# Kernel tuning notes

Hardware: AMD Instinct MI355X
Metric: run time of the kernel (lower is better)

## Reference

```python
import jax, jax.numpy as jnp
import numpy as np

# NF4 codebook (bitsandbytes normal-float-4 values)
NF4 = jnp.asarray(np.array([
    -1.0, -0.6961928009986877, -0.5250730514526367, -0.39491748809814453,
    -0.28444138169288635, -0.18477343022823334, -0.09105003625154495, 0.0,
    0.07958029955625534, 0.16093020141124725, 0.24611230194568634, 0.33791524171829224,
    0.44070982933044434, 0.5626170039176941, 0.7229568362236023, 1.0], dtype=np.float32))

BLOCK = 64         # bnb nf4 blocksize
SCALING = 2.0      # alpha / r = 128 / 64
OUT, IN = 4096, 4096

def dequantize_nf4(codes, absmax):
    # codes: [out, in] int32 in [0,16); absmax: [out*in/BLOCK] per-block scale
    vals = NF4[codes].reshape(-1, BLOCK)           # [n_blocks, BLOCK]
    w = vals * absmax[:, None]                     # blockwise rescale
    return w.reshape(OUT, IN)                      # [out, in]

def setup_inputs() -> dict:
    key = jax.random.key(0)
    k1, k2, k3, k4, k5 = jax.random.split(key, 5)
    x = jax.random.normal(k1, (4, 2048, 4096), dtype=jnp.float32)
    lora_A = jax.random.normal(k2, (64, 4096), dtype=jnp.float32) * 0.02
    lora_B = jax.random.normal(k3, (4096, 64), dtype=jnp.float32) * 0.02
    absmax = jax.random.uniform(k4, (4096 * 4096 // BLOCK,), dtype=jnp.float32) * 0.1
    qweight_codes = jax.random.randint(k5, (4096, 4096), 0, 16, dtype=jnp.int32)
    return {"x": x, "lora_A": lora_A, "lora_B": lora_B,
            "absmax": absmax, "qweight_codes": qweight_codes}

def reference(x, lora_A, lora_B, absmax, qweight_codes):
    # LinearForward, quantized nf4 path, no dora/bone, dropout disabled (eval):
    # F.linear(x, W) + scaling * F.linear(F.linear(x, lora_A), lora_B)
    W = dequantize_nf4(qweight_codes, absmax)              # [out, in]
    base = jnp.einsum('btd,od->bto', x, W)                 # base GEMM
    lora = jnp.einsum('btr,or->bto', jnp.einsum('btd,rd->btr', x, lora_A), lora_B)
    return base + SCALING * lora
```

## Files before the change

### kernel.cpp

```cpp
#include <hip/hip_runtime.h>


typedef _Float16 half8 __attribute__((ext_vector_type(8)));
typedef float f32x4 __attribute__((ext_vector_type(4)));

#define M_DIM 8192
#define N_DIM 4096
#define K_DIM 4096
#define NT (K_DIM / 64)

__constant__ float NF4C[16] = {
    -1.0f, -0.6961928009986877f, -0.5250730514526367f, -0.39491748809814453f,
    -0.28444138169288635f, -0.18477343022823334f, -0.09105003625154495f, 0.0f,
    0.07958029955625534f, 0.16093020141124725f, 0.24611230194568634f, 0.33791524171829224f,
    0.44070982933044434f, 0.5626170039176941f, 0.7229568362236023f, 1.0f};

__device__ __forceinline__ void gl16(void* lds_p, const void* g) {
  __builtin_amdgcn_global_load_lds(
      (const __attribute__((address_space(1))) void*)g,
      (__attribute__((address_space(3))) void*)lds_p, 16, 0, 0);
}

__global__ __launch_bounds__(256) void prep_x(const float4* __restrict__ x,
                                              half8* __restrict__ xh) {
  size_t i = (size_t)blockIdx.x * 256 + threadIdx.x;
  float4 a = x[2 * i];
  float4 b = x[2 * i + 1];
  half8 h;
  h[0] = (_Float16)a.x; h[1] = (_Float16)a.y; h[2] = (_Float16)a.z; h[3] = (_Float16)a.w;
  h[4] = (_Float16)b.x; h[5] = (_Float16)b.y; h[6] = (_Float16)b.z; h[7] = (_Float16)b.w;
  xh[i] = h;
}

#define PWP 132
__global__ __launch_bounds__(256) void prep_w(const float* __restrict__ lora_A,
                                              const float* __restrict__ lora_B,
                                              const float* __restrict__ absmax,
                                              const int* __restrict__ codes,
                                              _Float16* __restrict__ Wc) {
  __shared__ float At[64 * PWP];
  __shared__ float Bt[64 * PWP];
  __shared__ float nf4s[16];
  const int tid = threadIdx.x;
  const int bxi = blockIdx.x & 31;
  const int byo = blockIdx.x >> 5;
  const int i0 = bxi * 128;
  const int o0 = byo * 128;
  if (tid < 16) nf4s[tid] = NF4C[tid];
  for (int idx = tid; idx < 8192; idx += 256) {
    int r = idx >> 7, ii = idx & 127;
    At[r * PWP + ii] = lora_A[(size_t)r * 4096 + i0 + ii];
  }
  for (int idx = tid; idx < 8192; idx += 256) {
    int oo = idx >> 6, r = idx & 63;
    Bt[r * PWP + oo] = lora_B[(size_t)(o0 + oo) * 64 + r];
  }
  __syncthreads();
  const int tx = tid & 15;
  const int ty = tid >> 4;
  float accw[8][8];
#pragma unroll
  for (int i = 0; i < 8; ++i)
#pragma unroll
    for (int j = 0; j < 8; ++j) accw[i][j] = 0.0f;
  for (int r = 0; r < 64; ++r) {
    float4 a0 = *(const float4*)&At[r * PWP + tx * 8];
    float4 a1 = *(const float4*)&At[r * PWP + tx * 8 + 4];
    float4 b0 = *(const float4*)&Bt[r * PWP + ty * 8];
    float4 b1 = *(const float4*)&Bt[r * PWP + ty * 8 + 4];
    float av[8] = {a0.x, a0.y, a0.z, a0.w, a1.x, a1.y, a1.z, a1.w};
    float bv[8] = {b0.x, b0.y, b0.z, b0.w, b1.x, b1.y, b1.z, b1.w};
#pragma unroll
    for (int i = 0; i < 8; ++i)
#pragma unroll
      for (int j = 0; j < 8; ++j) accw[i][j] += bv[i] * av[j];
  }
#pragma unroll
  for (int i = 0; i < 8; ++i) {
    const int o_g = o0 + ty * 8 + i;
    const int* crow = codes + (size_t)o_g * 4096 + i0 + tx * 8;
    int4 c0 = *(const int4*)crow;
    int4 c1 = *(const int4*)(crow + 4);
    const float am = absmax[o_g * 64 + (i0 >> 6) + (tx >> 3)];
    half8 h;
    h[0] = (_Float16)(nf4s[c0.x] * am + 2.0f * accw[i][0]);
    h[1] = (_Float16)(nf4s[c0.y] * am + 2.0f * accw[i][1]);
    h[2] = (_Float16)(nf4s[c0.z] * am + 2.0f * accw[i][2]);
    h[3] = (_Float16)(nf4s[c0.w] * am + 2.0f * accw[i][3]);
    h[4] = (_Float16)(nf4s[c1.x] * am + 2.0f * accw[i][4]);
    h[5] = (_Float16)(nf4s[c1.y] * am + 2.0f * accw[i][5]);
    h[6] = (_Float16)(nf4s[c1.z] * am + 2.0f * accw[i][6]);
    h[7] = (_Float16)(nf4s[c1.w] * am + 2.0f * accw[i][7]);
    *(half8*)(Wc + (size_t)o_g * 4096 + i0 + tx * 8) = h;
  }
}


#define BAR __builtin_amdgcn_s_barrier()
#define PRIO1 __builtin_amdgcn_s_setprio(1)
#define PRIO0 __builtin_amdgcn_s_setprio(0)
#define SB0 __builtin_amdgcn_sched_barrier(0)

#define VMC_(N) asm volatile("s_waitcnt vmcnt(" #N ")" ::: "memory")
#define VMC(N) VMC_(N)
#define LG_(N)                                              \
  do {                                                      \
    asm volatile("s_waitcnt lgkmcnt(" #N ")" ::: "memory"); \
    __builtin_amdgcn_sched_barrier(0);                      \
  } while (0)
#define LG(N) LG_(N)

__global__ __launch_bounds__(512, 2) void gemm(const _Float16* __restrict__ Xh,
                                               const _Float16* __restrict__ Wc,
                                               float* __restrict__ out) {
  __shared__ _Float16 lds[65536];
  const int tid = threadIdx.x;
  const int lane = tid & 63;
  const int w = tid >> 6;

  const int swz = (blockIdx.x & 7) * 64 + (blockIdx.x >> 3);
  const int by = swz >> 4;
  const int bx = swz & 15;

  const int m16 = lane & 15;
  const int quad = lane >> 4;
  const int csw = (quad ^ (m16 & 7)) * 8;
  const int aoff0 = m16 * 64 + csw;
  const int aoff1 = m16 * 64 + (csw ^ 32);
  const int ha = w >> 2;
  const int hboff = ((w & 3) >> 1) * 8192 + (w & 1) * 4096;

  const int r0 = tid >> 3;
  const int lc = (tid & 7) ^ (r0 & 7);
  const _Float16* gAbase = Xh + (size_t)(by * 256 + r0) * K_DIM + lc * 8;
  const _Float16* gBbase = Wc + (size_t)(bx * 256 + r0) * K_DIM + lc * 8;

#define STAGE_A(H, BUF, T)                                                \
  do {                                                                    \
    _Float16* d_ = lds + (BUF) * 32768 + (H) * 8192 + w * 512;            \
    const _Float16* s_ = gAbase + (size_t)((H) * 128) * K_DIM + (T) * 64; \
    gl16(d_, s_);                                                         \
    gl16(d_ + 4096, s_ + (size_t)64 * K_DIM);                             \
  } while (0)
#define STAGE_B(H, BUF, T)                                                \
  do {                                                                    \
    _Float16* d_ = lds + (BUF) * 32768 + 16384 + (H) * 8192 + w * 512;    \
    const _Float16* s_ = gBbase + (size_t)((H) * 128) * K_DIM + (T) * 64; \
    gl16(d_, s_);                                                         \
    gl16(d_ + 4096, s_ + (size_t)64 * K_DIM);                             \
  } while (0)

  f32x4 acc[8][4];
#pragma unroll
  for (int m = 0; m < 8; ++m)
#pragma unroll
    for (int n = 0; n < 4; ++n) acc[m][n] = (f32x4){0.f, 0.f, 0.f, 0.f};

  half8 af[4][2];
  half8 bf[2][2];

#define RDA(FM, P)                                          \
  do {                                                      \
    af[FM][0] = *(const half8*)((P) + (FM)*1024 + aoff0);   \
    af[FM][1] = *(const half8*)((P) + (FM)*1024 + aoff1);   \
  } while (0)
#define RDB(FN, P)                                          \
  do {                                                      \
    bf[FN][0] = *(const half8*)((P) + (FN)*1024 + aoff0);   \
    bf[FN][1] = *(const half8*)((P) + (FN)*1024 + aoff1);   \
  } while (0)

#define MFM(FM, MH, NH)                                                      \
  do {                                                                       \
    acc[(MH)*4 + (FM)][(NH)*2 + 0] = __builtin_amdgcn_mfma_f32_16x16x32_f16( \
        af[FM][0], bf[0][0], acc[(MH)*4 + (FM)][(NH)*2 + 0], 0, 0, 0);       \
    acc[(MH)*4 + (FM)][(NH)*2 + 0] = __builtin_amdgcn_mfma_f32_16x16x32_f16( \
        af[FM][1], bf[0][1], acc[(MH)*4 + (FM)][(NH)*2 + 0], 0, 0, 0);       \
    acc[(MH)*4 + (FM)][(NH)*2 + 1] = __builtin_amdgcn_mfma_f32_16x16x32_f16( \
        af[FM][0], bf[1][0], acc[(MH)*4 + (FM)][(NH)*2 + 1], 0, 0, 0);       \
    acc[(MH)*4 + (FM)][(NH)*2 + 1] = __builtin_amdgcn_mfma_f32_16x16x32_f16( \
        af[FM][1], bf[1][1], acc[(MH)*4 + (FM)][(NH)*2 + 1], 0, 0, 0);       \
  } while (0)

#define MFN(FN, MH, NH)                                                          \
  do {                                                                           \
    _Pragma("unroll") for (int fm_ = 0; fm_ < 4; ++fm_) {                        \
      acc[(MH)*4 + fm_][(NH)*2 + (FN)] = __builtin_amdgcn_mfma_f32_16x16x32_f16( \
          af[fm_][0], bf[FN][0], acc[(MH)*4 + fm_][(NH)*2 + (FN)], 0, 0, 0);     \
      acc[(MH)*4 + fm_][(NH)*2 + (FN)] = __builtin_amdgcn_mfma_f32_16x16x32_f16( \
          af[fm_][1], bf[FN][1], acc[(MH)*4 + fm_][(NH)*2 + (FN)], 0, 0, 0);     \
    }                                                                            \
  } while (0)

#define TILE1(BUF, T, S)                                                \
  do {                                                                  \
    const _Float16* rA = lds + (BUF)*32768 + ha * 8192;                 \
    const _Float16* rB = lds + (BUF)*32768 + 16384 + hboff;             \
                   \
    RDB(0, rB); RDB(1, rB);                                             \
    RDA(0, rA); RDA(1, rA); RDA(2, rA); RDA(3, rA);                     \
    if (S) {                      \
      STAGE_A(0, (BUF) ^ 1, (T) + 1);                                   \
      STAGE_A(1, (BUF) ^ 1, (T) + 1);                                   \
      STAGE_B(0, (BUF) ^ 1, (T) + 1);                                   \
      STAGE_B(1, (BUF) ^ 1, (T) + 1);                                   \
    }                                                                   \
     \
    PRIO1;                                                              \
    LG(6); MFM(0, 0, 0);                             \
    LG(4); MFM(1, 0, 0);                                                \
    LG(2); MFM(2, 0, 0);                                                \
    LG(0); MFM(3, 0, 0);                                                \
    PRIO0;                                                              \
       \
    RDB(0, rB + 2048); RDB(1, rB + 2048);                               \
    PRIO1;                                                              \
    LG(2); MFN(0, 0, 1);                                                \
    LG(0); MFN(1, 0, 1);                                                \
    PRIO0;                                                              \
          \
    RDA(0, rA + 4096); RDA(1, rA + 4096);                               \
    RDA(2, rA + 4096); RDA(3, rA + 4096);                               \
    PRIO1;                                                              \
    LG(6); MFM(0, 1, 1);                                                \
    LG(4); MFM(1, 1, 1);                                                \
    LG(2); MFM(2, 1, 1);                                                \
    LG(0); MFM(3, 1, 1);                                                \
    PRIO0;                                                              \
        \
    RDB(0, rB); RDB(1, rB);                                             \
    PRIO1;                                                              \
    LG(2); MFN(0, 1, 0);                                                \
    LG(0); MFN(1, 1, 0);                                                \
    PRIO0;                                                              \
        \
    VMC(0);                                                             \
    BAR;                                                                \
  } while (0)

  STAGE_A(0, 0, 0);
  STAGE_A(1, 0, 0);
  STAGE_B(0, 0, 0);
  STAGE_B(1, 0, 0);
  VMC(0);
  BAR;

  for (int t2 = 0; t2 < NT - 2; t2 += 2) {
    TILE1(0, t2, 1);
    TILE1(1, t2 + 1, 1);
  }
  TILE1(0, NT - 2, 1);
  TILE1(1, NT - 1, 0);

  const size_t rowbase = (size_t)by * 256 + ha * 128 + quad * 4;
  const int colbase = bx * 256 + (w & 3) * 64 + m16;
#pragma unroll
  for (int m = 0; m < 8; ++m) {
#pragma unroll
    for (int r = 0; r < 4; ++r) {
      float* po = out + (rowbase + m * 16 + r) * N_DIM + colbase;
      po[0]  = acc[m][0][r];
      po[16] = acc[m][1][r];
      po[32] = acc[m][2][r];
      po[48] = acc[m][3][r];
    }
  }
}

extern "C" void kernel_launch(void* const* d_in, const int* in_sizes, int n_in,
                              void* d_out, int out_size, void* d_ws, size_t ws_size,
                              hipStream_t stream) {
  const float* x      = (const float*)d_in[0];
  const float* lora_A = (const float*)d_in[1];
  const float* lora_B = (const float*)d_in[2];
  const float* absmax = (const float*)d_in[3];
  const int*   codes  = (const int*)d_in[4];
  float* out = (float*)d_out;

  _Float16* Xh = (_Float16*)d_ws;
  _Float16* Wc = Xh + (size_t)M_DIM * K_DIM;

  hipLaunchKernelGGL(prep_x, dim3((M_DIM * K_DIM) / (8 * 256)), dim3(256), 0, stream,
                     (const float4*)x, (half8*)Xh);
  hipLaunchKernelGGL(prep_w, dim3((N_DIM / 128) * (K_DIM / 128)), dim3(256), 0, stream,
                     lora_A, lora_B, absmax, codes, Wc);
  hipLaunchKernelGGL(gemm, dim3((M_DIM / 256) * (N_DIM / 256)), dim3(512), 0, stream,
                     Xh, Wc, out);
}
```

Baseline: 534.6 us.

## Switch GEMM inner loop from 16x16x32 to 32x32x16 MFMA tiles

```diff
diff --git a/kernel.cpp b/kernel.cpp
--- a/kernel.cpp
+++ b/kernel.cpp
@@ -2,7 +2,7 @@
 
 
 typedef _Float16 half8 __attribute__((ext_vector_type(8)));
-typedef float f32x4 __attribute__((ext_vector_type(4)));
+typedef float f32x16 __attribute__((ext_vector_type(16)));
 
 #define M_DIM 8192
 #define N_DIM 4096
@@ -99,7 +99,6 @@
 #define BAR __builtin_amdgcn_s_barrier()
 #define PRIO1 __builtin_amdgcn_s_setprio(1)
 #define PRIO0 __builtin_amdgcn_s_setprio(0)
-#define SB0 __builtin_amdgcn_sched_barrier(0)
 
 #define VMC_(N) asm volatile("s_waitcnt vmcnt(" #N ")" ::: "memory")
 #define VMC(N) VMC_(N)
@@ -122,11 +121,14 @@
   const int by = swz >> 4;
   const int bx = swz & 15;
 
-  const int m16 = lane & 15;
-  const int quad = lane >> 4;
-  const int csw = (quad ^ (m16 & 7)) * 8;
-  const int aoff0 = m16 * 64 + csw;
-  const int aoff1 = m16 * 64 + (csw ^ 32);
+  const int l31 = lane & 31;
+  const int kh = lane >> 5;
+  const int rb = l31 & 7;
+  const int aro = l31 * 64;
+  const int ck0 = ((0 | kh) ^ rb) * 8;
+  const int ck1 = ((2 | kh) ^ rb) * 8;
+  const int ck2 = ((4 | kh) ^ rb) * 8;
+  const int ck3 = ((6 | kh) ^ rb) * 8;
   const int ha = w >> 2;
   const int hboff = ((w & 3) >> 1) * 8192 + (w & 1) * 4096;
 
@@ -150,92 +152,65 @@
     gl16(d_ + 4096, s_ + (size_t)64 * K_DIM);                             \
   } while (0)
 
-  f32x4 acc[8][4];
-#pragma unroll
-  for (int m = 0; m < 8; ++m)
-#pragma unroll
-    for (int n = 0; n < 4; ++n) acc[m][n] = (f32x4){0.f, 0.f, 0.f, 0.f};
-
-  half8 af[4][2];
-  half8 bf[2][2];
-
-#define RDA(FM, P)                                          \
+  f32x16 acc[4][2];
+#pragma unroll
+  for (int m = 0; m < 4; ++m)
+#pragma unroll
+    for (int n = 0; n < 2; ++n)
+#pragma unroll
+      for (int i = 0; i < 16; ++i) acc[m][n][i] = 0.0f;
+
+  half8 afA[4], bfA[2];
+  half8 afB[4], bfB[2];
+
+#define RDK(AF, BF, CK, rA, rB)                          \
+  do {                                                   \
+    AF[0] = *(const half8*)((rA) + aro + (CK));          \
+    AF[1] = *(const half8*)((rA) + 2048 + aro + (CK));   \
+    AF[2] = *(const half8*)((rA) + 4096 + aro + (CK));   \
+    AF[3] = *(const half8*)((rA) + 6144 + aro + (CK));   \
+    BF[0] = *(const half8*)((rB) + aro + (CK));          \
+    BF[1] = *(const half8*)((rB) + 2048 + aro + (CK));   \
+  } while (0)
+
+#define MFMA8(AF, BF)                                                       \
+  do {                                                                     \
+    PRIO1;                                                                 \
+    acc[0][0] = __builtin_amdgcn_mfma_f32_32x32x16_f16(AF[0], BF[0], acc[0][0], 0, 0, 0); \
+    acc[0][1] = __builtin_amdgcn_mfma_f32_32x32x16_f16(AF[0], BF[1], acc[0][1], 0, 0, 0); \
+    acc[1][0] = __builtin_amdgcn_mfma_f32_32x32x16_f16(AF[1], BF[0], acc[1][0], 0, 0, 0); \
+    acc[1][1] = __builtin_amdgcn_mfma_f32_32x32x16_f16(AF[1], BF[1], acc[1][1], 0, 0, 0); \
+    acc[2][0] = __builtin_amdgcn_mfma_f32_32x32x16_f16(AF[2], BF[0], acc[2][0], 0, 0, 0); \
+    acc[2][1] = __builtin_amdgcn_mfma_f32_32x32x16_f16(AF[2], BF[1], acc[2][1], 0, 0, 0); \
+    acc[3][0] = __builtin_amdgcn_mfma_f32_32x32x16_f16(AF[3], BF[0], acc[3][0], 0, 0, 0); \
+    acc[3][1] = __builtin_amdgcn_mfma_f32_32x32x16_f16(AF[3], BF[1], acc[3][1], 0, 0, 0); \
+    PRIO0;                                                                 \
+  } while (0)
+
+#define TILE32(BUF, T, S)                                   \
   do {                                                      \
-    af[FM][0] = *(const half8*)((P) + (FM)*1024 + aoff0);   \
-    af[FM][1] = *(const half8*)((P) + (FM)*1024 + aoff1);   \
-  } while (0)
-#define RDB(FN, P)                                          \
-  do {                                                      \
-    bf[FN][0] = *(const half8*)((P) + (FN)*1024 + aoff0);   \
-    bf[FN][1] = *(const half8*)((P) + (FN)*1024 + aoff1);   \
-  } while (0)
-
-#define MFM(FM, MH, NH)                                                      \
-  do {                                                                       \
-    acc[(MH)*4 + (FM)][(NH)*2 + 0] = __builtin_amdgcn_mfma_f32_16x16x32_f16( \
-        af[FM][0], bf[0][0], acc[(MH)*4 + (FM)][(NH)*2 + 0], 0, 0, 0);       \
-    acc[(MH)*4 + (FM)][(NH)*2 + 0] = __builtin_amdgcn_mfma_f32_16x16x32_f16( \
-        af[FM][1], bf[0][1], acc[(MH)*4 + (FM)][(NH)*2 + 0], 0, 0, 0);       \
-    acc[(MH)*4 + (FM)][(NH)*2 + 1] = __builtin_amdgcn_mfma_f32_16x16x32_f16( \
-        af[FM][0], bf[1][0], acc[(MH)*4 + (FM)][(NH)*2 + 1], 0, 0, 0);       \
-    acc[(MH)*4 + (FM)][(NH)*2 + 1] = __builtin_amdgcn_mfma_f32_16x16x32_f16( \
-        af[FM][1], bf[1][1], acc[(MH)*4 + (FM)][(NH)*2 + 1], 0, 0, 0);       \
-  } while (0)
-
-#define MFN(FN, MH, NH)                                                          \
-  do {                                                                           \
-    _Pragma("unroll") for (int fm_ = 0; fm_ < 4; ++fm_) {                        \
-      acc[(MH)*4 + fm_][(NH)*2 + (FN)] = __builtin_amdgcn_mfma_f32_16x16x32_f16( \
-          af[fm_][0], bf[FN][0], acc[(MH)*4 + fm_][(NH)*2 + (FN)], 0, 0, 0);     \
-      acc[(MH)*4 + fm_][(NH)*2 + (FN)] = __builtin_amdgcn_mfma_f32_16x16x32_f16( \
-          af[fm_][1], bf[FN][1], acc[(MH)*4 + fm_][(NH)*2 + (FN)], 0, 0, 0);     \
-    }                                                                            \
-  } while (0)
-
-#define TILE1(BUF, T, S)                                                \
-  do {                                                                  \
-    const _Float16* rA = lds + (BUF)*32768 + ha * 8192;                 \
-    const _Float16* rB = lds + (BUF)*32768 + 16384 + hboff;             \
-                   \
-    RDB(0, rB); RDB(1, rB);                                             \
-    RDA(0, rA); RDA(1, rA); RDA(2, rA); RDA(3, rA);                     \
-    if (S) {                      \
-      STAGE_A(0, (BUF) ^ 1, (T) + 1);                                   \
-      STAGE_A(1, (BUF) ^ 1, (T) + 1);                                   \
-      STAGE_B(0, (BUF) ^ 1, (T) + 1);                                   \
-      STAGE_B(1, (BUF) ^ 1, (T) + 1);                                   \
-    }                                                                   \
-     \
-    PRIO1;                                                              \
-    LG(6); MFM(0, 0, 0);                             \
-    LG(4); MFM(1, 0, 0);                                                \
-    LG(2); MFM(2, 0, 0);                                                \
-    LG(0); MFM(3, 0, 0);                                                \
-    PRIO0;                                                              \
-       \
-    RDB(0, rB + 2048); RDB(1, rB + 2048);                               \
-    PRIO1;                                                              \
-    LG(2); MFN(0, 0, 1);                                                \
-    LG(0); MFN(1, 0, 1);                                                \
-    PRIO0;                                                              \
-          \
-    RDA(0, rA + 4096); RDA(1, rA + 4096);                               \
-    RDA(2, rA + 4096); RDA(3, rA + 4096);                               \
-    PRIO1;                                                              \
-    LG(6); MFM(0, 1, 1);                                                \
-    LG(4); MFM(1, 1, 1);                                                \
-    LG(2); MFM(2, 1, 1);                                                \
-    LG(0); MFM(3, 1, 1);                                                \
-    PRIO0;                                                              \
-        \
-    RDB(0, rB); RDB(1, rB);                                             \
-    PRIO1;                                                              \
-    LG(2); MFN(0, 1, 0);                                                \
-    LG(0); MFN(1, 1, 0);                                                \
-    PRIO0;                                                              \
-        \
-    VMC(0);                                                             \
-    BAR;                                                                \
+    const _Float16* rA = lds + (BUF)*32768 + ha * 8192;     \
+    const _Float16* rB = lds + (BUF)*32768 + 16384 + hboff; \
+    RDK(afA, bfA, ck0, rA, rB);                             \
+    if (S) {                                                \
+      STAGE_A(0, (BUF) ^ 1, (T) + 1);                       \
+      STAGE_A(1, (BUF) ^ 1, (T) + 1);                       \
+      STAGE_B(0, (BUF) ^ 1, (T) + 1);                       \
+      STAGE_B(1, (BUF) ^ 1, (T) + 1);                       \
+    }                                                       \
+    RDK(afB, bfB, ck1, rA, rB);                             \
+    LG(6);                                                  \
+    MFMA8(afA, bfA);                                        \
+    RDK(afA, bfA, ck2, rA, rB);                             \
+    LG(6);                                                  \
+    MFMA8(afB, bfB);                                        \
+    RDK(afB, bfB, ck3, rA, rB);                             \
+    LG(6);                                                  \
+    MFMA8(afA, bfA);                                        \
+    LG(0);                                                  \
+    MFMA8(afB, bfB);                                        \
+    VMC(0);                                                 \
+    BAR;                                                    \
   } while (0)
 
   STAGE_A(0, 0, 0);
@@ -246,23 +221,23 @@
   BAR;
 
   for (int t2 = 0; t2 < NT - 2; t2 += 2) {
-    TILE1(0, t2, 1);
-    TILE1(1, t2 + 1, 1);
-  }
-  TILE1(0, NT - 2, 1);
-  TILE1(1, NT - 1, 0);
-
-  const size_t rowbase = (size_t)by * 256 + ha * 128 + quad * 4;
-  const int colbase = bx * 256 + (w & 3) * 64 + m16;
-#pragma unroll
-  for (int m = 0; m < 8; ++m) {
-#pragma unroll
-    for (int r = 0; r < 4; ++r) {
-      float* po = out + (rowbase + m * 16 + r) * N_DIM + colbase;
-      po[0]  = acc[m][0][r];
-      po[16] = acc[m][1][r];
-      po[32] = acc[m][2][r];
-      po[48] = acc[m][3][r];
+    TILE32(0, t2, 1);
+    TILE32(1, t2 + 1, 1);
+  }
+  TILE32(0, NT - 2, 1);
+  TILE32(1, NT - 1, 0);
+
+  const size_t rowbase = (size_t)by * 256 + ha * 128 + 4 * kh;
+  const int colbase = bx * 256 + (w & 3) * 64 + l31;
+#pragma unroll
+  for (int mt = 0; mt < 4; ++mt) {
+#pragma unroll
+    for (int nt = 0; nt < 2; ++nt) {
+#pragma unroll
+      for (int i = 0; i < 16; ++i) {
+        const size_t row = rowbase + mt * 32 + (i & 3) + 8 * (i >> 2);
+        out[row * N_DIM + colbase + nt * 32] = acc[mt][nt][i];
+      }
     }
   }
 }
```

New measurement: 548.6 us. 2.6% more time.
